# Kernel optimization log

Hardware: AMD Instinct MI355X
Metric: run time of the kernel (lower is better)

## Reference

```python
import jax, jax.numpy as jnp
import numpy as np

D_MODEL = 256
N_HEADS = 8
N_LEVELS = 4
N_POINTS = 4
D_FFN = 1024
HW = 128
LQ = HW * HW
LIN = N_LEVELS * LQ
BATCH = 2
HEAD_DIM = D_MODEL // N_HEADS
SPATIAL = [(HW, HW)] * N_LEVELS  # static (H, W) per level
EPS = 1e-5


def _layer_norm(x, g, b):
    m = jnp.mean(x, axis=-1, keepdims=True)
    v = jnp.mean(jnp.square(x - m), axis=-1, keepdims=True)
    return (x - m) * jax.lax.rsqrt(v + EPS) * g + b


def _gather(v, idx):
    # v: (N, heads, HW, hd); idx: (N, heads, Lq, P) -> (N, heads, Lq, P, hd)
    N, Hh, Lq, P = idx.shape
    out = jnp.take_along_axis(v, idx.reshape(N, Hh, Lq * P)[..., None], axis=2)
    return out.reshape(N, Hh, Lq, P, -1)


def _ms_deform_attn_core(value, loc, attn):
    # value: (N, Lin, heads, hd); loc: (N, Lq, heads, L, P, 2) in [0,1]; attn: (N, Lq, heads, L, P)
    N, _, Hh, hd = value.shape
    Lq = loc.shape[1]
    out = jnp.zeros((N, Hh, Lq, hd), value.dtype)
    start = 0
    for l, (H, W) in enumerate(SPATIAL):
        v = value[:, start:start + H * W].transpose(0, 2, 1, 3)  # (N, heads, H*W, hd)
        start += H * W
        ll = loc[:, :, :, l].transpose(0, 2, 1, 3, 4)  # (N, heads, Lq, P, 2)
        # F.grid_sample(align_corners=False, padding_mode='zeros') on grid 2*loc-1:
        # pixel coord = loc * size - 0.5
        x = ll[..., 0] * W - 0.5
        y = ll[..., 1] * H - 0.5
        x0 = jnp.floor(x)
        y0 = jnp.floor(y)
        wx = x - x0
        wy = y - y0
        x0i = x0.astype(jnp.int32)
        y0i = y0.astype(jnp.int32)
        acc = jnp.zeros((N, Hh, Lq, N_POINTS, hd), value.dtype)
        for dy, wyc in ((0, 1.0 - wy), (1, wy)):
            for dx, wxc in ((0, 1.0 - wx), (1, wx)):
                xi = x0i + dx
                yi = y0i + dy
                valid = (xi >= 0) & (xi < W) & (yi >= 0) & (yi < H)
                idx = jnp.clip(yi, 0, H - 1) * W + jnp.clip(xi, 0, W - 1)
                g = _gather(v, idx)
                w = (wxc * wyc * valid).astype(value.dtype)
                acc = acc + g * w[..., None]
        aw = attn[:, :, :, l].transpose(0, 2, 1, 3)  # (N, heads, Lq, P)
        out = out + jnp.sum(acc * aw[..., None], axis=3)
    return out.transpose(0, 2, 1, 3).reshape(N, Lq, Hh * hd)


def _forward(cur_src, src_all, pos, reference_points, spatial_shape,
             W_off, b_off, W_attn, b_attn, W_val, b_val, W_out, b_out,
             gamma1, beta1, W1, b1, W2, b2, gamma2, beta2):
    N, Lq, d = cur_src.shape
    q = cur_src + pos[:, -1]                      # with_pos_embed(cur_src, pos[-1])
    inp = src_all + pos.reshape(N, -1, d)         # with_pos_embed(src_all, cat(pos, 1))
    value = (inp @ W_val + b_val).reshape(N, -1, N_HEADS, HEAD_DIM)
    off = (q @ W_off + b_off).reshape(N, Lq, N_HEADS, N_LEVELS, N_POINTS, 2)
    attn = (q @ W_attn + b_attn).reshape(N, Lq, N_HEADS, N_LEVELS * N_POINTS)
    attn = jax.nn.softmax(attn, axis=-1).reshape(N, Lq, N_HEADS, N_LEVELS, N_POINTS)
    # offset_normalizer = stack([W, H], -1)
    normalizer = jnp.stack([spatial_shape[..., 1], spatial_shape[..., 0]], -1).astype(cur_src.dtype)
    loc = reference_points[:, :, None, :, None, :] + off / normalizer[None, None, None, :, None, :]
    src2 = _ms_deform_attn_core(value, loc, attn) @ W_out + b_out
    src = _layer_norm(cur_src + src2, gamma1, beta1)   # dropout is identity in eval
    ffn = jax.nn.relu(src @ W1 + b1) @ W2 + b2
    return _layer_norm(src + ffn, gamma2, beta2)


def setup_inputs():
    key = jax.random.key(0)
    ks = jax.random.split(key, 16)
    s = 0.02
    f32 = jnp.float32
    return {
        "cur_src": jax.random.normal(ks[0], (BATCH, LQ, D_MODEL), f32),
        "src_all": jax.random.normal(ks[1], (BATCH, LIN, D_MODEL), f32),
        "pos": jax.random.normal(ks[2], (BATCH, N_LEVELS, LQ, D_MODEL), f32),
        "reference_points": jax.random.uniform(ks[3], (BATCH, LQ, N_LEVELS, 2), f32),
        "spatial_shape": jnp.array(SPATIAL, dtype=jnp.int32),
        "level_start_index": (jnp.arange(N_LEVELS) * LQ).astype(jnp.int32),
        "W_off": jax.random.normal(ks[4], (D_MODEL, N_HEADS * N_LEVELS * N_POINTS * 2), f32) * s,
        "b_off": jax.random.normal(ks[5], (N_HEADS * N_LEVELS * N_POINTS * 2,), f32) * 0.5,
        "W_attn": jax.random.normal(ks[6], (D_MODEL, N_HEADS * N_LEVELS * N_POINTS), f32) * s,
        "b_attn": jnp.zeros((N_HEADS * N_LEVELS * N_POINTS,), f32),
        "W_val": jax.random.normal(ks[7], (D_MODEL, D_MODEL), f32) * s,
        "b_val": jnp.zeros((D_MODEL,), f32),
        "W_out": jax.random.normal(ks[8], (D_MODEL, D_MODEL), f32) * s,
        "b_out": jnp.zeros((D_MODEL,), f32),
        "gamma1": jnp.ones((D_MODEL,), f32),
        "beta1": jnp.zeros((D_MODEL,), f32),
        "W1": jax.random.normal(ks[9], (D_MODEL, D_FFN), f32) * s,
        "b1": jnp.zeros((D_FFN,), f32),
        "W2": jax.random.normal(ks[10], (D_FFN, D_MODEL), f32) * s,
        "b2": jnp.zeros((D_MODEL,), f32),
        "gamma2": jnp.ones((D_MODEL,), f32),
        "beta2": jnp.zeros((D_MODEL,), f32),
    }


def reference(cur_src, src_all, pos, reference_points, spatial_shape, level_start_index,
              W_off, b_off, W_attn, b_attn, W_val, b_val, W_out, b_out,
              gamma1, beta1, W1, b1, W2, b2, gamma2, beta2):
    return _forward(cur_src, src_all, pos, reference_points, spatial_shape,
                    W_off, b_off, W_attn, b_attn, W_val, b_val, W_out, b_out,
                    gamma1, beta1, W1, b1, W2, b2, gamma2, beta2)
```

## Files before the change

### kernel.cpp

```cpp
#include <hip/hip_runtime.h>

#define LQN   16384
#define LINN  65536

typedef __attribute__((ext_vector_type(8))) short bf16x8;
typedef __attribute__((ext_vector_type(4))) float f32x4;
typedef __attribute__((ext_vector_type(4))) unsigned short bf16x4;

__device__ __forceinline__ unsigned short f2bf(float f) {
  unsigned u = __float_as_uint(f);
  u += 0x7FFFu + ((u >> 16) & 1u);
  return (unsigned short)(u >> 16);
}
__device__ __forceinline__ unsigned pk2bf(float lo, float hi) {
  return (unsigned)f2bf(lo) | ((unsigned)f2bf(hi) << 16);
}

__global__ __launch_bounds__(256) void wtrans6_kernel(
    const float* __restrict__ Wv, const float* __restrict__ Wo,
    const float* __restrict__ Wa, const float* __restrict__ Wu,
    const float* __restrict__ W1, const float* __restrict__ W2,
    unsigned short* __restrict__ wt) {
  int idx = blockIdx.x * 256 + threadIdx.x;
  const float* W; int K, N, base;
  if (idx < 131072) {
    if (idx < 65536) { W = Wv; K = 256; N = 256; base = 0; }
    else             { W = Wo; K = 256; N = 256; base = 65536; }
  } else if (idx < 229376) {
    if (idx < 163840) { W = Wa; K = 256; N = 128; base = 131072; }
    else              { W = Wu; K = 256; N = 256; base = 163840; }
  } else if (idx < 491520) { W = W1; K = 256; N = 1024; base = 229376; }
  else                     { W = W2; K = 1024; N = 256; base = 491520; }
  int local = idx - base;
  int n = local / K, k = local - n * K;
  wt[idx] = f2bf(W[(size_t)k * N + n]);
}

__global__ __launch_bounds__(256) void addcvt_q_kernel(
    const float* __restrict__ cur, const float* __restrict__ pos,
    unsigned short* __restrict__ qb) {
  size_t j = (size_t)blockIdx.x * 256 + threadIdx.x;
  size_t row = j >> 6;
  int n = (int)(row >> 14), lq = (int)(row & 16383);
  float4 a = ((const float4*)cur)[j];
  float4 b = ((const float4*)pos)[(((size_t)n * 4 + 3) * LQN + lq) * 64 + (j & 63)];
  bf16x4 o;
  o.x = f2bf(a.x + b.x); o.y = f2bf(a.y + b.y);
  o.z = f2bf(a.z + b.z); o.w = f2bf(a.w + b.w);
  ((bf16x4*)qb)[j] = o;
}

__global__ __launch_bounds__(512) void gemmv_fused_kernel(
    const float* __restrict__ SA, const float* __restrict__ PS,
    const unsigned short* __restrict__ Bt, const float* __restrict__ bias,
    unsigned short* __restrict__ Cp) {
  __shared__ unsigned short As[128 * 64];
  __shared__ unsigned short Bs[256 * 64];
  const int m0 = blockIdx.x * 128;
  const int tid = threadIdx.x;
  const int wave = tid >> 6, lane = tid & 63;
  const int wm = (wave >> 2) * 64;
  const int wn = (wave & 3) * 64;
  const int l15 = lane & 15, quad = lane >> 4;
  const int rl = lane >> 3;
  const int cl = (lane & 7) ^ rl;

  const int ar = wave * 16 + (lane >> 2);
  const int cb = (lane & 3) * 2;
  const float* pa = SA + (size_t)(m0 + ar) * 256 + cb * 8;
  const float* pb = PS + (size_t)(m0 + ar) * 256 + cb * 8;

  const unsigned short* Bbase = Bt + cl * 8;

  f32x4 acc[4][4];
#pragma unroll
  for (int i = 0; i < 4; i++)
#pragma unroll
    for (int j = 0; j < 4; j++)
#pragma unroll
      for (int r = 0; r < 4; r++) acc[i][j][r] = 0.f;

  for (int k0 = 0; k0 < 256; k0 += 64) {
#pragma unroll
    for (int t = 0; t < 4; t++) {
      const int row = wave * 32 + t * 8 + rl;
      __builtin_amdgcn_global_load_lds(
          (const __attribute__((address_space(1))) void*)(Bbase + (size_t)row * 256 + k0),
          (__attribute__((address_space(3))) void*)(Bs + (wave * 32 + t * 8) * 64),
          16, 0, 0);
    }
    float4 fa[4], fb[4];
#pragma unroll
    for (int u = 0; u < 4; u++) fa[u] = ((const float4*)(pa + k0))[u];
#pragma unroll
    for (int u = 0; u < 4; u++) fb[u] = ((const float4*)(pb + k0))[u];
#pragma unroll
    for (int c = 0; c < 2; c++) {
      uint4 wv;
      wv.x = pk2bf(fa[2 * c].x + fb[2 * c].x, fa[2 * c].y + fb[2 * c].y);
      wv.y = pk2bf(fa[2 * c].z + fb[2 * c].z, fa[2 * c].w + fb[2 * c].w);
      wv.z = pk2bf(fa[2 * c + 1].x + fb[2 * c + 1].x, fa[2 * c + 1].y + fb[2 * c + 1].y);
      wv.w = pk2bf(fa[2 * c + 1].z + fb[2 * c + 1].z, fa[2 * c + 1].w + fb[2 * c + 1].w);
      const int p = (cb + c) ^ (ar & 7);
      *(uint4*)((char*)As + ar * 128 + p * 16) = wv;
    }
    __syncthreads();
#pragma unroll
    for (int kk = 0; kk < 2; kk++) {
      bf16x8 af[4], bfr[4];
#pragma unroll
      for (int i = 0; i < 4; i++) {
        const int row = wm + i * 16 + l15;
        af[i] = *(const bf16x8*)&As[row * 64 + (((quad + 4 * kk) ^ (row & 7)) * 8)];
      }
#pragma unroll
      for (int j = 0; j < 4; j++) {
        const int row = wn + j * 16 + l15;
        bfr[j] = *(const bf16x8*)&Bs[row * 64 + (((quad + 4 * kk) ^ (row & 7)) * 8)];
      }
#pragma unroll
      for (int i = 0; i < 4; i++)
#pragma unroll
        for (int j = 0; j < 4; j++)
          acc[i][j] = __builtin_amdgcn_mfma_f32_16x16x32_bf16(af[i], bfr[j], acc[i][j], 0, 0, 0);
    }
    __syncthreads();
  }
#pragma unroll
  for (int i = 0; i < 4; i++) {
#pragma unroll
    for (int j = 0; j < 4; j++) {
      const int col = wn + j * 16 + l15;
      const float bv = bias[col];
#pragma unroll
      for (int r = 0; r < 4; r++) {
        const int row = m0 + wm + i * 16 + quad * 4 + r;
        const float v = acc[i][j][r] + bv;
        const size_t addr = (((size_t)(row >> 16) * 8 + (col >> 5)) * 65536 +
                             (size_t)(row & 65535)) * 32 + (col & 31);
        Cp[addr] = f2bf(v);
      }
    }
  }
}

template <int DO_RELU, int OUT_BF16, int SPLIT>
__global__ __launch_bounds__(256) void gemm_lds_kernel(
    const unsigned short* __restrict__ A, const unsigned short* __restrict__ Bt,
    const float* __restrict__ bias, const float* __restrict__ bias2,
    void* __restrict__ Cp, float* __restrict__ Cp2,
    int M, int N, int K, int ny) {
  __shared__ unsigned short As[128 * 64];
  __shared__ unsigned short Bs[128 * 64];
  const int bid = blockIdx.x;
  const int by = bid % ny, bx = bid / ny;
  const int m0 = bx * 128, n0 = by * 128;
  const int tid = threadIdx.x;
  const int wave = tid >> 6, lane = tid & 63;
  const int wm = (wave >> 1) * 64, wn = (wave & 1) * 64;
  const int l15 = lane & 15, quad = lane >> 4;
  const int rl = lane >> 3;
  const int cl = (lane & 7) ^ rl;

  f32x4 acc[4][4];
#pragma unroll
  for (int i = 0; i < 4; i++)
#pragma unroll
    for (int j = 0; j < 4; j++)
#pragma unroll
      for (int r = 0; r < 4; r++) acc[i][j][r] = 0.f;

  const unsigned short* Abase = A + (size_t)m0 * K + cl * 8;
  const unsigned short* Bbase = Bt + (size_t)n0 * K + cl * 8;

  for (int k0 = 0; k0 < K; k0 += 64) {
#pragma unroll
    for (int t = 0; t < 4; t++) {
      const int row = wave * 32 + t * 8 + rl;
      __builtin_amdgcn_global_load_lds(
          (const __attribute__((address_space(1))) void*)(Abase + (size_t)row * K + k0),
          (__attribute__((address_space(3))) void*)(As + (wave * 32 + t * 8) * 64),
          16, 0, 0);
      __builtin_amdgcn_global_load_lds(
          (const __attribute__((address_space(1))) void*)(Bbase + (size_t)row * K + k0),
          (__attribute__((address_space(3))) void*)(Bs + (wave * 32 + t * 8) * 64),
          16, 0, 0);
    }
    __syncthreads();
#pragma unroll
    for (int kk = 0; kk < 2; kk++) {
      bf16x8 af[4], bfr[4];
#pragma unroll
      for (int i = 0; i < 4; i++) {
        const int row = wm + i * 16 + l15;
        af[i] = *(const bf16x8*)&As[row * 64 + (((quad + 4 * kk) ^ (row & 7)) * 8)];
      }
#pragma unroll
      for (int j = 0; j < 4; j++) {
        const int row = wn + j * 16 + l15;
        bfr[j] = *(const bf16x8*)&Bs[row * 64 + (((quad + 4 * kk) ^ (row & 7)) * 8)];
      }
#pragma unroll
      for (int i = 0; i < 4; i++)
#pragma unroll
        for (int j = 0; j < 4; j++)
          acc[i][j] = __builtin_amdgcn_mfma_f32_16x16x32_bf16(af[i], bfr[j], acc[i][j], 0, 0, 0);
    }
    __syncthreads();
  }
#pragma unroll
  for (int i = 0; i < 4; i++) {
#pragma unroll
    for (int j = 0; j < 4; j++) {
      const int col = n0 + wn + j * 16 + l15;
      float bv;
      if (SPLIT) bv = (col < 256) ? bias[col] : bias2[col - 256];
      else       bv = bias[col];
#pragma unroll
      for (int r = 0; r < 4; r++) {
        const int row = m0 + wm + i * 16 + quad * 4 + r;
        float v = acc[i][j][r] + bv;
        if (DO_RELU) v = fmaxf(v, 0.f);
        if (SPLIT) {
          if (col < 256) ((float*)Cp)[(size_t)row * 256 + col] = v;
          else           Cp2[(size_t)row * 128 + (col - 256)] = v;
        } else if (OUT_BF16) {
          ((unsigned short*)Cp)[(size_t)row * N + col] = f2bf(v);
        } else {
          ((float*)Cp)[(size_t)row * N + col] = v;
        }
      }
    }
  }
}

__global__ __launch_bounds__(256) void sample_kernel(
    const unsigned short* __restrict__ value, const float* __restrict__ offs,
    const float* __restrict__ attnl, const float* __restrict__ refp,
    unsigned int* __restrict__ attn_out) {
  __shared__ float wlds[32][132];
  const int tid = threadIdx.x;
  const int sub = tid >> 3;
  const int cl  = tid & 7;
  const int gb = blockIdx.x * 32 + sub;
  const int h  = gb >> 15;
  const int nl = gb & 32767;
  const int n  = nl >> 14;
  const int g  = nl * 8 + h;

  const float* lg = attnl + (size_t)nl * 128 + h * 16;
  const float2 l2 = *(const float2*)(lg + 2 * cl);
  float mx = fmaxf(l2.x, l2.y);
#pragma unroll
  for (int o = 1; o < 8; o <<= 1) mx = fmaxf(mx, __shfl_xor(mx, o, 8));
  const float e0 = __expf(l2.x - mx), e1 = __expf(l2.y - mx);
  float s = e0 + e1;
#pragma unroll
  for (int o = 1; o < 8; o <<= 1) s += __shfl_xor(s, o, 8);
  const float inv = 1.f / s;

  const float4 o4 = *(const float4*)(offs + (size_t)g * 32 + 4 * cl);
  const float2 r2 = *(const float2*)(refp + ((size_t)nl * 4 + (cl >> 1)) * 2);
#pragma unroll
  for (int q = 0; q < 2; q++) {
    const float ox = (q == 0) ? o4.x : o4.z;
    const float oy = (q == 0) ? o4.y : o4.w;
    const float aw = ((q == 0) ? e0 : e1) * inv;
    const float x = fmaf(r2.x, 128.f, ox - 0.5f);
    const float y = fmaf(r2.y, 128.f, oy - 0.5f);
    const float xf = floorf(x), yf = floorf(y);
    const float fx = x - xf, fy = y - yf;
    const int x0 = (int)xf, y0 = (int)yf;
    const float wx0 = (x0 >= 0 && x0 <= 127) ? (1.f - fx) : 0.f;
    const float wx1 = (x0 >= -1 && x0 <= 126) ? fx : 0.f;
    const float wy0 = ((y0 >= 0 && y0 <= 127) ? (1.f - fy) : 0.f) * aw;
    const float wy1 = ((y0 >= -1 && y0 <= 126) ? fy : 0.f) * aw;
    const int px = min(max(x0, 0), 126);
    const float wl = (px == x0) ? wx0 : ((px == x0 + 1) ? wx1 : 0.f);
    const float wr = (px + 1 == x0) ? wx0 : ((px == x0) ? wx1 : 0.f);
    const int yc0 = min(max(y0, 0), 127), yc1 = min(max(y0 + 1, 0), 127);
    const int lb = (cl >> 1) * 16384;
    const unsigned ot = (unsigned)(lb + yc0 * 128 + px) * 64u;
    const unsigned ob = (unsigned)(lb + yc1 * 128 + px) * 64u;
    float* wp = &wlds[sub][(2 * cl + q) * 8];
    wp[0] = wl * wy0; wp[1] = wr * wy0;
    wp[2] = wl * wy1; wp[3] = wr * wy1;
    wp[4] = __uint_as_float(ot); wp[5] = __uint_as_float(ob);
  }

  const char* hb = (const char*)value + (((size_t)(n * 8 + h)) << 22) + cl * 16;
  float a0 = 0.f, a1 = 0.f, a2 = 0.f, a3 = 0.f;
  float a4 = 0.f, a5 = 0.f, a6 = 0.f, a7 = 0.f;
#pragma unroll
  for (int p = 0; p < 16; p++) {
    const float4 w4 = *(const float4*)&wlds[sub][p * 8];
    const float2 of2 = *(const float2*)&wlds[sub][p * 8 + 4];
    const uint4 vt = *(const uint4*)(hb + __float_as_uint(of2.x));
    const uint4 vb = *(const uint4*)(hb + __float_as_uint(of2.y));
    const float wtop = (cl < 4) ? w4.x : w4.y;
    const float wbot = (cl < 4) ? w4.z : w4.w;
#define ACC8(vv, wgt)                                              \
    a0 = fmaf(wgt, __uint_as_float((vv).x << 16), a0);             \
    a1 = fmaf(wgt, __uint_as_float((vv).x & 0xFFFF0000u), a1);     \
    a2 = fmaf(wgt, __uint_as_float((vv).y << 16), a2);             \
    a3 = fmaf(wgt, __uint_as_float((vv).y & 0xFFFF0000u), a3);     \
    a4 = fmaf(wgt, __uint_as_float((vv).z << 16), a4);             \
    a5 = fmaf(wgt, __uint_as_float((vv).z & 0xFFFF0000u), a5);     \
    a6 = fmaf(wgt, __uint_as_float((vv).w << 16), a6);             \
    a7 = fmaf(wgt, __uint_as_float((vv).w & 0xFFFF0000u), a7);
    ACC8(vt, wtop)
    ACC8(vb, wbot)
#undef ACC8
  }
  a0 += __shfl_xor(a0, 4, 8); a1 += __shfl_xor(a1, 4, 8);
  a2 += __shfl_xor(a2, 4, 8); a3 += __shfl_xor(a3, 4, 8);
  a4 += __shfl_xor(a4, 4, 8); a5 += __shfl_xor(a5, 4, 8);
  a6 += __shfl_xor(a6, 4, 8); a7 += __shfl_xor(a7, 4, 8);
  if (cl < 4) {
    uint4 o;
    o.x = (unsigned)f2bf(a0) | ((unsigned)f2bf(a1) << 16);
    o.y = (unsigned)f2bf(a2) | ((unsigned)f2bf(a3) << 16);
    o.z = (unsigned)f2bf(a4) | ((unsigned)f2bf(a5) << 16);
    o.w = (unsigned)f2bf(a6) | ((unsigned)f2bf(a7) << 16);
    ((uint4*)attn_out)[(size_t)g * 4 + cl] = o;
  }
}

template <int EMIT_BF16>
__global__ __launch_bounds__(256) void ln_kernel(const float* __restrict__ x1,
                                                 const float* __restrict__ x2,
                                                 const float* __restrict__ gamma,
                                                 const float* __restrict__ beta,
                                                 float* __restrict__ out,
                                                 unsigned short* __restrict__ outb) {
  const int row = blockIdx.x * 4 + (threadIdx.x >> 6);
  const int lane = threadIdx.x & 63;
  float4 a = ((const float4*)(x1 + (size_t)row * 256))[lane];
  float4 b = ((const float4*)(x2 + (size_t)row * 256))[lane];
  float v0 = a.x + b.x, v1 = a.y + b.y, v2 = a.z + b.z, v3 = a.w + b.w;
  float s1 = v0 + v1 + v2 + v3;
  float s2 = v0 * v0 + v1 * v1 + v2 * v2 + v3 * v3;
#pragma unroll
  for (int o = 1; o < 64; o <<= 1) { s1 += __shfl_xor(s1, o); s2 += __shfl_xor(s2, o); }
  const float mean = s1 * (1.f / 256.f);
  const float var = s2 * (1.f / 256.f) - mean * mean;
  const float rstd = rsqrtf(var + 1e-5f);
  float4 gm = ((const float4*)gamma)[lane];
  float4 bt = ((const float4*)beta)[lane];
  float4 o4;
  o4.x = (v0 - mean) * rstd * gm.x + bt.x;
  o4.y = (v1 - mean) * rstd * gm.y + bt.y;
  o4.z = (v2 - mean) * rstd * gm.z + bt.z;
  o4.w = (v3 - mean) * rstd * gm.w + bt.w;
  ((float4*)(out + (size_t)row * 256))[lane] = o4;
  if (EMIT_BF16) {
    bf16x4 ob;
    ob.x = f2bf(o4.x); ob.y = f2bf(o4.y); ob.z = f2bf(o4.z); ob.w = f2bf(o4.w);
    ((bf16x4*)(outb + (size_t)row * 256))[lane] = ob;
  }
}

extern "C" void kernel_launch(void* const* d_in, const int* in_sizes, int n_in,
                              void* d_out, int out_size, void* d_ws, size_t ws_size,
                              hipStream_t stream) {
  (void)in_sizes; (void)n_in; (void)out_size; (void)ws_size;
  const float* cur_src = (const float*)d_in[0];
  const float* src_all = (const float*)d_in[1];
  const float* pos     = (const float*)d_in[2];
  const float* refp    = (const float*)d_in[3];
  const float* W_off   = (const float*)d_in[6];
  const float* b_off   = (const float*)d_in[7];
  const float* W_attn  = (const float*)d_in[8];
  const float* b_attn  = (const float*)d_in[9];
  const float* W_val   = (const float*)d_in[10];
  const float* b_val   = (const float*)d_in[11];
  const float* W_out   = (const float*)d_in[12];
  const float* b_out   = (const float*)d_in[13];
  const float* gamma1  = (const float*)d_in[14];
  const float* beta1   = (const float*)d_in[15];
  const float* W1      = (const float*)d_in[16];
  const float* b1      = (const float*)d_in[17];
  const float* W2      = (const float*)d_in[18];
  const float* b2      = (const float*)d_in[19];
  const float* gamma2  = (const float*)d_in[20];
  const float* beta2   = (const float*)d_in[21];
  float* out = (float*)d_out;

  char* ws = (char*)d_ws;
  unsigned short* value = (unsigned short*)(ws + 0);
  unsigned short* qbuf  = (unsigned short*)(ws + 67108864);
  float* offbuf         = (float*)(ws + 83886080);
  float* attnl          = (float*)(ws + 117440512);
  unsigned short* attno = (unsigned short*)(ws + 134217728);
  float* src2           = (float*)(ws + 150994944);
  float* srcb           = (float*)(ws + 184549376);
  unsigned short* wt    = (unsigned short*)(ws + 218103808);
  unsigned short* wt_val  = wt;
  unsigned short* wt_qa   = wt + 65536;
  unsigned short* wt_out  = wt + 163840;
  unsigned short* wt_1    = wt + 229376;
  unsigned short* wt_2    = wt + 491520;
  unsigned short* srcb_bf = (unsigned short*)attnl;

  wtrans6_kernel<<<2944, 256, 0, stream>>>(W_val, W_off, W_attn, W_out, W1, W2, wt);

  addcvt_q_kernel<<<8192, 256, 0, stream>>>(cur_src, pos, qbuf);

  gemmv_fused_kernel<<<1024, 512, 0, stream>>>(src_all, pos, wt_val, b_val, value);

  gemm_lds_kernel<0, 0, 1><<<768, 256, 0, stream>>>(
      qbuf, wt_qa, b_off, b_attn, offbuf, attnl, 32768, 384, 256, 3);
  sample_kernel<<<8192, 256, 0, stream>>>(value, offbuf, attnl, refp,
                                          (unsigned int*)attno);
  gemm_lds_kernel<0, 0, 0><<<512, 256, 0, stream>>>(
      attno, wt_out, b_out, nullptr, src2, nullptr, 32768, 256, 256, 2);
  ln_kernel<1><<<8192, 256, 0, stream>>>(cur_src, src2, gamma1, beta1, srcb, srcb_bf);
  gemm_lds_kernel<1, 1, 0><<<2048, 256, 0, stream>>>(
      srcb_bf, wt_1, b1, nullptr, value, nullptr, 32768, 1024, 256, 8);
  gemm_lds_kernel<0, 0, 0><<<512, 256, 0, stream>>>(
      value, wt_2, b2, nullptr, offbuf, nullptr, 32768, 256, 1024, 2);
  ln_kernel<0><<<8192, 256, 0, stream>>>(srcb, offbuf, gamma2, beta2, out, nullptr);
}
```

Before: 605.9 us.

## Fuse output and FFN2 GEMMs with residual LayerNorm; shrink value GEMM tile

Adds a GEMM kernel with a 128x256 tile that covers full 256-wide rows. It adds bias and residual and computes LayerNorm in the epilogue, reducing row statistics through shuffles and LDS. This replaces two GEMM+LN kernel pairs and removes the fp32 intermediate round trips through global memory and two launches. The value-projection GEMM tile is also halved to 64 rows, doubling its grid for more parallelism. The cost is only 256 blocks for the fused GEMMs, which may underfill the GPU, and uncoalesced scalar stores in the epilogue.

```diff
diff --git a/kernel.cpp b/kernel.cpp
--- a/kernel.cpp
+++ b/kernel.cpp
@@ -54,27 +54,26 @@
     const float* __restrict__ SA, const float* __restrict__ PS,
     const unsigned short* __restrict__ Bt, const float* __restrict__ bias,
     unsigned short* __restrict__ Cp) {
-  __shared__ unsigned short As[128 * 64];
+  __shared__ unsigned short As[64 * 64];
   __shared__ unsigned short Bs[256 * 64];
-  const int m0 = blockIdx.x * 128;
+  const int m0 = blockIdx.x * 64;
   const int tid = threadIdx.x;
   const int wave = tid >> 6, lane = tid & 63;
-  const int wm = (wave >> 2) * 64;
+  const int wm = (wave >> 2) * 32;
   const int wn = (wave & 3) * 64;
   const int l15 = lane & 15, quad = lane >> 4;
   const int rl = lane >> 3;
   const int cl = (lane & 7) ^ rl;
 
-  const int ar = wave * 16 + (lane >> 2);
-  const int cb = (lane & 3) * 2;
-  const float* pa = SA + (size_t)(m0 + ar) * 256 + cb * 8;
-  const float* pb = PS + (size_t)(m0 + ar) * 256 + cb * 8;
-
+  const int ar = tid >> 3;
+  const int sub = tid & 7;
+  const float* pa = SA + (size_t)(m0 + ar) * 256 + sub * 8;
+  const float* pb = PS + (size_t)(m0 + ar) * 256 + sub * 8;
   const unsigned short* Bbase = Bt + cl * 8;
 
-  f32x4 acc[4][4];
-#pragma unroll
-  for (int i = 0; i < 4; i++)
+  f32x4 acc[2][4];
+#pragma unroll
+  for (int i = 0; i < 2; i++)
 #pragma unroll
     for (int j = 0; j < 4; j++)
 #pragma unroll
@@ -89,27 +88,23 @@
           (__attribute__((address_space(3))) void*)(Bs + (wave * 32 + t * 8) * 64),
           16, 0, 0);
     }
-    float4 fa[4], fb[4];
-#pragma unroll
-    for (int u = 0; u < 4; u++) fa[u] = ((const float4*)(pa + k0))[u];
-#pragma unroll
-    for (int u = 0; u < 4; u++) fb[u] = ((const float4*)(pb + k0))[u];
-#pragma unroll
-    for (int c = 0; c < 2; c++) {
-      uint4 wv;
-      wv.x = pk2bf(fa[2 * c].x + fb[2 * c].x, fa[2 * c].y + fb[2 * c].y);
-      wv.y = pk2bf(fa[2 * c].z + fb[2 * c].z, fa[2 * c].w + fb[2 * c].w);
-      wv.z = pk2bf(fa[2 * c + 1].x + fb[2 * c + 1].x, fa[2 * c + 1].y + fb[2 * c + 1].y);
-      wv.w = pk2bf(fa[2 * c + 1].z + fb[2 * c + 1].z, fa[2 * c + 1].w + fb[2 * c + 1].w);
-      const int p = (cb + c) ^ (ar & 7);
-      *(uint4*)((char*)As + ar * 128 + p * 16) = wv;
-    }
+    float4 fa0 = ((const float4*)(pa + k0))[0];
+    float4 fa1 = ((const float4*)(pa + k0))[1];
+    float4 fb0 = ((const float4*)(pb + k0))[0];
+    float4 fb1 = ((const float4*)(pb + k0))[1];
+    uint4 wv;
+    wv.x = pk2bf(fa0.x + fb0.x, fa0.y + fb0.y);
+    wv.y = pk2bf(fa0.z + fb0.z, fa0.w + fb0.w);
+    wv.z = pk2bf(fa1.x + fb1.x, fa1.y + fb1.y);
+    wv.w = pk2bf(fa1.z + fb1.z, fa1.w + fb1.w);
+    const int p = sub ^ (ar & 7);
+    *(uint4*)((char*)As + ar * 128 + p * 16) = wv;
     __syncthreads();
 #pragma unroll
     for (int kk = 0; kk < 2; kk++) {
-      bf16x8 af[4], bfr[4];
-#pragma unroll
-      for (int i = 0; i < 4; i++) {
+      bf16x8 af[2], bfr[4];
+#pragma unroll
+      for (int i = 0; i < 2; i++) {
         const int row = wm + i * 16 + l15;
         af[i] = *(const bf16x8*)&As[row * 64 + (((quad + 4 * kk) ^ (row & 7)) * 8)];
       }
@@ -119,7 +114,7 @@
         bfr[j] = *(const bf16x8*)&Bs[row * 64 + (((quad + 4 * kk) ^ (row & 7)) * 8)];
       }
 #pragma unroll
-      for (int i = 0; i < 4; i++)
+      for (int i = 0; i < 2; i++)
 #pragma unroll
         for (int j = 0; j < 4; j++)
           acc[i][j] = __builtin_amdgcn_mfma_f32_16x16x32_bf16(af[i], bfr[j], acc[i][j], 0, 0, 0);
@@ -127,7 +122,7 @@
     __syncthreads();
   }
 #pragma unroll
-  for (int i = 0; i < 4; i++) {
+  for (int i = 0; i < 2; i++) {
 #pragma unroll
     for (int j = 0; j < 4; j++) {
       const int col = wn + j * 16 + l15;
@@ -229,6 +224,139 @@
         } else {
           ((float*)Cp)[(size_t)row * N + col] = v;
         }
+      }
+    }
+  }
+}
+
+template <int EMIT_BF16>
+__global__ __launch_bounds__(512) void gemm_ln_kernel(
+    const unsigned short* __restrict__ A, const unsigned short* __restrict__ Bt,
+    const float* __restrict__ bias, const float* __restrict__ res,
+    const float* __restrict__ gamma, const float* __restrict__ beta,
+    float* __restrict__ outf, unsigned short* __restrict__ outb, int K) {
+  __shared__ unsigned short As[128 * 64];
+  __shared__ unsigned short Bs[256 * 64];
+  __shared__ float lnred[128][4];
+  __shared__ float lnsq[128][4];
+  const int m0 = blockIdx.x * 128;
+  const int tid = threadIdx.x;
+  const int wave = tid >> 6, lane = tid & 63;
+  const int wm = (wave >> 2) * 64;
+  const int wn = (wave & 3) * 64;
+  const int l15 = lane & 15, quad = lane >> 4;
+  const int rl = lane >> 3;
+  const int cl = (lane & 7) ^ rl;
+
+  f32x4 acc[4][4];
+#pragma unroll
+  for (int i = 0; i < 4; i++)
+#pragma unroll
+    for (int j = 0; j < 4; j++)
+#pragma unroll
+      for (int r = 0; r < 4; r++) acc[i][j][r] = 0.f;
+
+  const unsigned short* Abase = A + (size_t)m0 * K + cl * 8;
+  const unsigned short* Bbase = Bt + cl * 8;
+
+  for (int k0 = 0; k0 < K; k0 += 64) {
+#pragma unroll
+    for (int t = 0; t < 2; t++) {
+      const int row = wave * 16 + t * 8 + rl;
+      __builtin_amdgcn_global_load_lds(
+          (const __attribute__((address_space(1))) void*)(Abase + (size_t)row * K + k0),
+          (__attribute__((address_space(3))) void*)(As + (wave * 16 + t * 8) * 64),
+          16, 0, 0);
+    }
+#pragma unroll
+    for (int t = 0; t < 4; t++) {
+      const int row = wave * 32 + t * 8 + rl;
+      __builtin_amdgcn_global_load_lds(
+          (const __attribute__((address_space(1))) void*)(Bbase + (size_t)row * K + k0),
+          (__attribute__((address_space(3))) void*)(Bs + (wave * 32 + t * 8) * 64),
+          16, 0, 0);
+    }
+    __syncthreads();
+#pragma unroll
+    for (int kk = 0; kk < 2; kk++) {
+      bf16x8 af[4], bfr[4];
+#pragma unroll
+      for (int i = 0; i < 4; i++) {
+        const int row = wm + i * 16 + l15;
+        af[i] = *(const bf16x8*)&As[row * 64 + (((quad + 4 * kk) ^ (row & 7)) * 8)];
+      }
+#pragma unroll
+      for (int j = 0; j < 4; j++) {
+        const int row = wn + j * 16 + l15;
+        bfr[j] = *(const bf16x8*)&Bs[row * 64 + (((quad + 4 * kk) ^ (row & 7)) * 8)];
+      }
+#pragma unroll
+      for (int i = 0; i < 4; i++)
+#pragma unroll
+        for (int j = 0; j < 4; j++)
+          acc[i][j] = __builtin_amdgcn_mfma_f32_16x16x32_bf16(af[i], bfr[j], acc[i][j], 0, 0, 0);
+    }
+    __syncthreads();
+  }
+
+  float s1[4][4], s2[4][4];
+#pragma unroll
+  for (int i = 0; i < 4; i++)
+#pragma unroll
+    for (int r = 0; r < 4; r++) { s1[i][r] = 0.f; s2[i][r] = 0.f; }
+#pragma unroll
+  for (int i = 0; i < 4; i++) {
+#pragma unroll
+    for (int j = 0; j < 4; j++) {
+      const int col = wn + j * 16 + l15;
+      const float bv = bias[col];
+#pragma unroll
+      for (int r = 0; r < 4; r++) {
+        const int rloc = wm + i * 16 + quad * 4 + r;
+        const size_t grow = (size_t)(m0 + rloc);
+        float u = acc[i][j][r] + bv + res[grow * 256 + col];
+        acc[i][j][r] = u;
+        s1[i][r] += u; s2[i][r] += u * u;
+      }
+    }
+  }
+#pragma unroll
+  for (int o = 1; o < 16; o <<= 1) {
+#pragma unroll
+    for (int i = 0; i < 4; i++)
+#pragma unroll
+      for (int r = 0; r < 4; r++) {
+        s1[i][r] += __shfl_xor(s1[i][r], o);
+        s2[i][r] += __shfl_xor(s2[i][r], o);
+      }
+  }
+  if (l15 == 0) {
+#pragma unroll
+    for (int i = 0; i < 4; i++)
+#pragma unroll
+      for (int r = 0; r < 4; r++) {
+        const int rloc = wm + i * 16 + quad * 4 + r;
+        lnred[rloc][wave & 3] = s1[i][r];
+        lnsq[rloc][wave & 3] = s2[i][r];
+      }
+  }
+  __syncthreads();
+#pragma unroll
+  for (int i = 0; i < 4; i++) {
+#pragma unroll
+    for (int r = 0; r < 4; r++) {
+      const int rloc = wm + i * 16 + quad * 4 + r;
+      const float S1 = lnred[rloc][0] + lnred[rloc][1] + lnred[rloc][2] + lnred[rloc][3];
+      const float S2 = lnsq[rloc][0] + lnsq[rloc][1] + lnsq[rloc][2] + lnsq[rloc][3];
+      const float mean = S1 * (1.f / 256.f);
+      const float rstd = rsqrtf(S2 * (1.f / 256.f) - mean * mean + 1e-5f);
+      const size_t grow = (size_t)(m0 + rloc);
+#pragma unroll
+      for (int j = 0; j < 4; j++) {
+        const int col = wn + j * 16 + l15;
+        const float o = (acc[i][j][r] - mean) * rstd * gamma[col] + beta[col];
+        outf[grow * 256 + col] = o;
+        if (EMIT_BF16) outb[grow * 256 + col] = f2bf(o);
       }
     }
   }
@@ -323,40 +451,6 @@
     o.z = (unsigned)f2bf(a4) | ((unsigned)f2bf(a5) << 16);
     o.w = (unsigned)f2bf(a6) | ((unsigned)f2bf(a7) << 16);
     ((uint4*)attn_out)[(size_t)g * 4 + cl] = o;
-  }
-}
-
-template <int EMIT_BF16>
-__global__ __launch_bounds__(256) void ln_kernel(const float* __restrict__ x1,
-                                                 const float* __restrict__ x2,
-                                                 const float* __restrict__ gamma,
-                                                 const float* __restrict__ beta,
-                                                 float* __restrict__ out,
-                                                 unsigned short* __restrict__ outb) {
-  const int row = blockIdx.x * 4 + (threadIdx.x >> 6);
-  const int lane = threadIdx.x & 63;
-  float4 a = ((const float4*)(x1 + (size_t)row * 256))[lane];
-  float4 b = ((const float4*)(x2 + (size_t)row * 256))[lane];
-  float v0 = a.x + b.x, v1 = a.y + b.y, v2 = a.z + b.z, v3 = a.w + b.w;
-  float s1 = v0 + v1 + v2 + v3;
-  float s2 = v0 * v0 + v1 * v1 + v2 * v2 + v3 * v3;
-#pragma unroll
-  for (int o = 1; o < 64; o <<= 1) { s1 += __shfl_xor(s1, o); s2 += __shfl_xor(s2, o); }
-  const float mean = s1 * (1.f / 256.f);
-  const float var = s2 * (1.f / 256.f) - mean * mean;
-  const float rstd = rsqrtf(var + 1e-5f);
-  float4 gm = ((const float4*)gamma)[lane];
-  float4 bt = ((const float4*)beta)[lane];
-  float4 o4;
-  o4.x = (v0 - mean) * rstd * gm.x + bt.x;
-  o4.y = (v1 - mean) * rstd * gm.y + bt.y;
-  o4.z = (v2 - mean) * rstd * gm.z + bt.z;
-  o4.w = (v3 - mean) * rstd * gm.w + bt.w;
-  ((float4*)(out + (size_t)row * 256))[lane] = o4;
-  if (EMIT_BF16) {
-    bf16x4 ob;
-    ob.x = f2bf(o4.x); ob.y = f2bf(o4.y); ob.z = f2bf(o4.z); ob.w = f2bf(o4.w);
-    ((bf16x4*)(outb + (size_t)row * 256))[lane] = ob;
   }
 }
 
@@ -392,7 +486,6 @@
   float* offbuf         = (float*)(ws + 83886080);
   float* attnl          = (float*)(ws + 117440512);
   unsigned short* attno = (unsigned short*)(ws + 134217728);
-  float* src2           = (float*)(ws + 150994944);
   float* srcb           = (float*)(ws + 184549376);
   unsigned short* wt    = (unsigned short*)(ws + 218103808);
   unsigned short* wt_val  = wt;
@@ -406,18 +499,16 @@
 
   addcvt_q_kernel<<<8192, 256, 0, stream>>>(cur_src, pos, qbuf);
 
-  gemmv_fused_kernel<<<1024, 512, 0, stream>>>(src_all, pos, wt_val, b_val, value);
+  gemmv_fused_kernel<<<2048, 512, 0, stream>>>(src_all, pos, wt_val, b_val, value);
 
   gemm_lds_kernel<0, 0, 1><<<768, 256, 0, stream>>>(
       qbuf, wt_qa, b_off, b_attn, offbuf, attnl, 32768, 384, 256, 3);
   sample_kernel<<<8192, 256, 0, stream>>>(value, offbuf, attnl, refp,
                                           (unsigned int*)attno);
-  gemm_lds_kernel<0, 0, 0><<<512, 256, 0, stream>>>(
-      attno, wt_out, b_out, nullptr, src2, nullptr, 32768, 256, 256, 2);
-  ln_kernel<1><<<8192, 256, 0, stream>>>(cur_src, src2, gamma1, beta1, srcb, srcb_bf);
+  gemm_ln_kernel<1><<<256, 512, 0, stream>>>(
+      attno, wt_out, b_out, cur_src, gamma1, beta1, srcb, srcb_bf, 256);
   gemm_lds_kernel<1, 1, 0><<<2048, 256, 0, stream>>>(
       srcb_bf, wt_1, b1, nullptr, value, nullptr, 32768, 1024, 256, 8);
-  gemm_lds_kernel<0, 0, 0><<<512, 256, 0, stream>>>(
-      value, wt_2, b2, nullptr, offbuf, nullptr, 32768, 256, 1024, 2);
-  ln_kernel<0><<<8192, 256, 0, stream>>>(srcb, offbuf, gamma2, beta2, out, nullptr);
-}
+  gemm_ln_kernel<0><<<256, 512, 0, stream>>>(
+      value, wt_2, b2, srcb, gamma2, beta2, out, nullptr, 1024);
+}
```

Result: faster. 584.1 us (-3.6%).
